# Performance work log

Hardware: AMD Instinct MI355X
Metric: run time of the kernel (lower is better)

## Reference

```python
import jax, jax.numpy as jnp
import numpy as np

B, N, C, NC = 16, 49, 512, 12  # batch, spatial tokens, channels, num AU classes
EPS = 1e-5


def bn(h, axes):
    # torch BatchNorm (training mode, gamma=1, beta=0): biased batch stats
    m = h.mean(axes, keepdims=True)
    v = h.var(axes, keepdims=True)
    return (h - m) * jax.lax.rsqrt(v + EPS)


def cross_attn(y, x, qw, qb, kw, kb, vw, vb):
    # CrossAttn: q from y, k/v from x; attention over the token (N) axis
    q = y @ qw.T + qb            # (..., N, C//2)
    k = x @ kw.T + kb
    v = x @ vw.T + vb            # (..., N, C)
    scale = (C // 2) ** -0.5
    attn = jax.nn.softmax(jnp.einsum('...ij,...kj->...ik', q, k) * scale, axis=-1)
    return attn @ v


def _gnn_block(x, edge, A, Bm, E, U, V):
    # One ME-GraphAU GCN message-passing block.
    # x: (B, NC, C) node feats; edge: (B, NC*NC, C), edge (i,j) stored at i*NC+j
    b = x.shape[0]
    Vix = x @ A.T   # gathered at end node j of each edge
    Vjx = x @ Bm.T  # gathered at start node i of each edge
    msg = (Vjx[:, :, None, :] + Vix[:, None, :, :]).reshape(b, NC * NC, C) + edge @ E.T
    edge = edge + jax.nn.relu(bn(msg, (0, 2)))              # bne: per-edge-slot stats
    e = jax.nn.sigmoid(edge).reshape(b, NC, NC, C)
    e = jax.nn.softmax(e, axis=2)                            # softmax over target j
    Ujx = x @ V.T                                            # start-node features
    agg = (e * Ujx[:, :, None, :]).sum(axis=1) / NC          # sum over source i -> node j
    xn = x @ U.T + agg
    x = jax.nn.relu(x + bn(xn, (0, 2)))                      # bnv: per-class stats
    return x, edge


def _forward(x, cls_w, cls_b, attn_qw, attn_qb, attn_kw, attn_kb, attn_vw, attn_vb,
             ep_w, ep_b, gnn_w, mlp_w1, mlp_b1, mlp_w2, mlp_b2, mlp_w3, mlp_b3,
             final_w, final_b):
    b = x.shape[0]
    # per-class LinearBlocks, batched: (B, NC, N, C)
    h = jnp.einsum('bnc,koc->bkno', x, cls_w) + cls_b[None, :, None, :]
    f_u = jax.nn.relu(bn(h, (0, 2)))           # each class has its own BN over (B, N)
    f_v = f_u.mean(-2)                          # (B, NC, C)

    # GEM edge extractor
    g = jnp.broadcast_to(x[:, None], (b, NC, N, C))
    feat = cross_attn(f_u, g, attn_qw[0], attn_qb[0], attn_kw[0], attn_kb[0], attn_vw[0], attn_vb[0])
    # feat_end[i*NC+j] = feat[i]; feat_start[i*NC+j] = feat[j]
    feat_end = jnp.broadcast_to(feat[:, :, None], (b, NC, NC, N, C)).reshape(b, NC * NC, N, C)
    feat_start = jnp.broadcast_to(feat[:, None, :], (b, NC, NC, N, C)).reshape(b, NC * NC, N, C)
    feat2 = cross_attn(feat_start, feat_end, attn_qw[1], attn_qb[1], attn_kw[1], attn_kb[1], attn_vw[1], attn_vb[1])
    edge = bn(feat2 @ ep_w.T + ep_b, (0, 2, 3))  # BatchNorm2d(NC*NC): stats over (B, N, C)
    f_e = edge.mean(-2)                           # (B, NC*NC, C)

    # two GCN message-passing blocks
    U1, V1, A1, B1, E1, U2, V2, A2, B2, E2 = gnn_w
    f_v, f_e = _gnn_block(f_v, f_e, A1, B1, E1, U1, V1)
    f_v, f_e = _gnn_block(f_v, f_e, A2, B2, E2, U2, V2)

    # vectorized pairwise class-link head (feed_type='vertex+edge'), pairs i<j in loop order
    iu, ju = np.triu_indices(NC, 1)
    edges = jnp.concatenate([f_e[:, iu * NC + ju], f_e[:, ju * NC + iu]], axis=-1)  # (B, 66, 2C)
    nodes = jnp.concatenate([f_v[:, iu], f_v[:, ju]], axis=-1)                       # (B, 66, 2C)

    def mlp(z, i):
        z = jax.nn.relu(z @ mlp_w1[i].T + mlp_b1[i])
        z = jax.nn.relu(z @ mlp_w2[i].T + mlp_b2[i])
        return z @ mlp_w3[i].T + mlp_b3[i]

    ed = mlp(edges, 0)
    nd = mlp(nodes, 1)
    return jnp.concatenate([ed, nd], axis=-1) @ final_w.T + final_b  # (B, 66, 4)


def setup_inputs() -> dict:
    key = jax.random.key(0)
    ks = jax.random.split(key, 12)

    def w(k, shape, fan_in):
        return jax.random.normal(k, shape, jnp.float32) * (2.0 / fan_in) ** 0.5

    return dict(
        x=jax.random.normal(ks[0], (B, N, C), jnp.float32),
        cls_w=w(ks[1], (NC, C, C), C),          # per-class Linear (out, in)
        cls_b=jnp.zeros((NC, C), jnp.float32),
        attn_qw=w(ks[2], (2, C // 2, C), C),    # [0]=FAM, [1]=ARM
        attn_qb=jnp.zeros((2, C // 2), jnp.float32),
        attn_kw=w(ks[3], (2, C // 2, C), C),
        attn_kb=jnp.zeros((2, C // 2), jnp.float32),
        attn_vw=w(ks[4], (2, C, C), C),
        attn_vb=jnp.zeros((2, C), jnp.float32),
        ep_w=w(ks[5], (C, C), C),               # GEM edge_proj
        ep_b=jnp.zeros((C,), jnp.float32),
        gnn_w=w(ks[6], (10, C, C), C),          # U1,V1,A1,B1,E1,U2,V2,A2,B2,E2 (no bias)
        mlp_w1=w(ks[7], (2, C, 2 * C), 2 * C),  # [0]=edge_fc_*, [1]=node_fc_*
        mlp_b1=jnp.zeros((2, C), jnp.float32),
        mlp_w2=w(ks[8], (2, C // 2, C), C),
        mlp_b2=jnp.zeros((2, C // 2), jnp.float32),
        mlp_w3=w(ks[9], (2, 4, C // 2), C // 2),
        mlp_b3=jnp.zeros((2, 4), jnp.float32),
        final_w=w(ks[10], (4, 8), 8),
        final_b=jnp.zeros((4,), jnp.float32),
    )


def reference(x, cls_w, cls_b, attn_qw, attn_qb, attn_kw, attn_kb, attn_vw, attn_vb,
              ep_w, ep_b, gnn_w, mlp_w1, mlp_b1, mlp_w2, mlp_b2, mlp_w3, mlp_b3,
              final_w, final_b):
    return _forward(x, cls_w, cls_b, attn_qw, attn_qb, attn_kw, attn_kb, attn_vw, attn_vb,
                    ep_w, ep_b, gnn_w, mlp_w1, mlp_b1, mlp_w2, mlp_b2, mlp_w3, mlp_b3,
                    final_w, final_b)
```

## Files before the change

kernel.cpp:

```cpp
#include <hip/hip_runtime.h>

#define BN_EPS 1e-5f

typedef float f32x4 __attribute__((ext_vector_type(4)));
typedef short s16x8 __attribute__((ext_vector_type(8)));

__device__ __forceinline__ short f2bf(float f) {
    unsigned u = __builtin_bit_cast(unsigned, f);
    u = (u + 0x7fffu + ((u >> 16) & 1u)) >> 16;
    return (short)u;
}

__global__ __launch_bounds__(256) void cvt_multi_kernel(
    const float* __restrict__ s0, const float* __restrict__ s1, const float* __restrict__ s2,
    const float* __restrict__ s3, const float* __restrict__ s4, const float* __restrict__ s5,
    const float* __restrict__ s6, const float* __restrict__ s7, const float* __restrict__ s8,
    short* __restrict__ d0, short* __restrict__ d1, short* __restrict__ d2,
    short* __restrict__ d3, short* __restrict__ d4, short* __restrict__ d5,
    short* __restrict__ d6, short* __restrict__ d7, short* __restrict__ d8)
{
    int idx = blockIdx.x * 256 + threadIdx.x;
    const float* src; short* dst; int local;
    if      (idx <   50176) { src = s0; dst = d0; local = idx; }
    else if (idx <  443392) { src = s1; dst = d1; local = idx -   50176; }
    else if (idx <  476160) { src = s2; dst = d2; local = idx -  443392; }
    else if (idx <  508928) { src = s3; dst = d3; local = idx -  476160; }
    else if (idx <  574464) { src = s4; dst = d4; local = idx -  508928; }
    else if (idx <  607232) { src = s5; dst = d5; local = idx -  574464; }
    else if (idx <  934912) { src = s6; dst = d6; local = idx -  607232; }
    else if (idx < 1065984) { src = s7; dst = d7; local = idx -  934912; }
    else if (idx < 1098752) { src = s8; dst = d8; local = idx - 1065984; }
    else return;
    const float4* s4p = reinterpret_cast<const float4*>(src) + (size_t)local * 2;
    float4 a = s4p[0], b = s4p[1];
    s16x8 v;
    v[0] = f2bf(a.x); v[1] = f2bf(a.y); v[2] = f2bf(a.z); v[3] = f2bf(a.w);
    v[4] = f2bf(b.x); v[5] = f2bf(b.y); v[6] = f2bf(b.z); v[7] = f2bf(b.w);
    reinterpret_cast<s16x8*>(dst)[local] = v;
}

template<int OMODE>
__global__ __launch_bounds__(256) void mfma_linear_kernel(
    const short* __restrict__ X, int Xstride,
    const short* __restrict__ W, int Wstride,
    const float* __restrict__ bias, int bstride,
    void* __restrict__ Yv, int Ystride,
    int R, int Cin, int Cout, int relu)
{
    const int mat = blockIdx.z;
    X += (size_t)mat * Xstride;
    W += (size_t)mat * Wstride;
    const float* bp = bias ? bias + mat * bstride : nullptr;
    float* Yf = (float*)Yv + (size_t)mat * Ystride;
    short* Ys = (short*)Yv + (size_t)mat * Ystride;

    const int r0 = blockIdx.y * 64;
    const int o0 = blockIdx.x * 64;

    __shared__ short As[64 * 40];
    __shared__ short Bs[64 * 40];

    const int tid = threadIdx.x;
    const int lane = tid & 63;
    const int wave = tid >> 6;
    const int wr = wave >> 1, wc = wave & 1;
    const int l15 = lane & 15;
    const int lk = lane >> 4;

    const int trow = tid >> 2;
    const int tseg = (tid & 3) * 8;

    f32x4 acc[2][2] = {};

    const int arow = r0 + trow;
    const bool aok = arow < R;
    const short* xrow = X + (size_t)arow * Cin + tseg;
    const short* wrow = W + (size_t)(o0 + trow) * Cin + tseg;

    for (int k0 = 0; k0 < Cin; k0 += 32) {
        s16x8 av = {};
        if (aok) av = *reinterpret_cast<const s16x8*>(xrow + k0);
        s16x8 bv = *reinterpret_cast<const s16x8*>(wrow + k0);
        *reinterpret_cast<s16x8*>(&As[trow * 40 + tseg]) = av;
        *reinterpret_cast<s16x8*>(&Bs[trow * 40 + tseg]) = bv;
        __syncthreads();

        s16x8 af[2], bf[2];
        #pragma unroll
        for (int mi = 0; mi < 2; mi++)
            af[mi] = *reinterpret_cast<const s16x8*>(&As[(wr * 32 + mi * 16 + l15) * 40 + lk * 8]);
        #pragma unroll
        for (int ni = 0; ni < 2; ni++)
            bf[ni] = *reinterpret_cast<const s16x8*>(&Bs[(wc * 32 + ni * 16 + l15) * 40 + lk * 8]);
        #pragma unroll
        for (int mi = 0; mi < 2; mi++)
            #pragma unroll
            for (int ni = 0; ni < 2; ni++)
                acc[mi][ni] = __builtin_amdgcn_mfma_f32_16x16x32_bf16(af[mi], bf[ni], acc[mi][ni], 0, 0, 0);
        __syncthreads();
    }

    #pragma unroll
    for (int mi = 0; mi < 2; mi++) {
        #pragma unroll
        for (int ni = 0; ni < 2; ni++) {
            int col = o0 + wc * 32 + ni * 16 + l15;
            int row0 = r0 + wr * 32 + mi * 16 + lk * 4;
            float bb = bp ? bp[col] : 0.f;
            #pragma unroll
            for (int r = 0; r < 4; r++) {
                int row = row0 + r;
                if (row < R) {
                    float v = acc[mi][ni][r] + bb;
                    if (relu) v = fmaxf(v, 0.f);
                    if (OMODE == 0) {
                        Yf[(size_t)row * Cout + col] = v;
                    } else if (OMODE == 1) {
                        Ys[(size_t)row * Cout + col] = f2bf(v);
                    } else {
                        int t = row / 49, n = row - t * 49;
                        Ys[((size_t)t * 512 + col) * 64 + n] = f2bf(v);
                    }
                }
            }
        }
    }
}

__global__ __launch_bounds__(256) void bn1_partial_kernel(
    const float* __restrict__ h, float* __restrict__ bsum, float* __restrict__ bsq)
{
    int k = blockIdx.x;
    int part = blockIdx.y;
    int tid = threadIdx.x;
    #pragma unroll
    for (int half = 0; half < 2; half++) {
        int o = tid + half * 256;
        const float* base = h + (size_t)k * 401408 + (size_t)part * 98 * 512 + o;
        float s = 0.f, sq = 0.f;
        #pragma unroll 7
        for (int bn = 0; bn < 98; bn++) {
            float v = base[bn * 512];
            s += v; sq += v * v;
        }
        atomicAdd(&bsum[k * 512 + o], s);
        atomicAdd(&bsq[k * 512 + o], sq);
    }
}

__global__ __launch_bounds__(256) void fu_fv_kernel(
    const float* __restrict__ h, const float* __restrict__ bsum,
    const float* __restrict__ bsq, short* __restrict__ fu_bf,
    float* __restrict__ f_v, short* __restrict__ fv_bf)
{
    int b = blockIdx.x;
    int k = blockIdx.y;
    int tid = threadIdx.x;
    #pragma unroll
    for (int half = 0; half < 2; half++) {
        int o = tid + half * 256;
        float mu = bsum[k * 512 + o] * (1.f / 784.f);
        float var = bsq[k * 512 + o] * (1.f / 784.f) - mu * mu;
        float rs = rsqrtf(var + BN_EPS);
        const float* base = h + (size_t)(k * 16 + b) * 49 * 512 + o;
        short* obase = fu_bf + (size_t)(k * 16 + b) * 49 * 512 + o;
        float acc = 0.f;
        #pragma unroll 7
        for (int n = 0; n < 49; n++) {
            float v = (base[n * 512] - mu) * rs;
            v = fmaxf(v, 0.f);
            obase[n * 512] = f2bf(v);
            acc += v;
        }
        float fvv = acc * (1.f / 49.f);
        f_v[(b * 12 + k) * 512 + o] = fvv;
        fv_bf[(b * 12 + k) * 512 + o] = f2bf(fvv);
    }
}

__global__ __launch_bounds__(256) void attn1_mfma_kernel(
    const short* __restrict__ q1,
    const short* __restrict__ k1,
    const short* __restrict__ v1T,
    short* __restrict__ feat)
{
    const int b = blockIdx.x, k = blockIdx.y;
    __shared__ float S[64 * 68];
    __shared__ short P[64 * 88];
    const int tid = threadIdx.x;
    const int lane = tid & 63, w = tid >> 6;
    const int l15 = lane & 15, lk = lane >> 4;

    for (int idx = tid; idx < 64 * 88; idx += 256) P[idx] = 0;
    const short* qb = q1 + (size_t)((k * 16 + b) * 49) * 256;
    const short* kb = k1 + (size_t)(b * 49) * 256;
    __syncthreads();

    {
        int qrow = w * 16 + l15; if (qrow > 48) qrow = 48;
        f32x4 sacc[4] = {};
        #pragma unroll
        for (int ks = 0; ks < 8; ks++) {
            s16x8 aq = *reinterpret_cast<const s16x8*>(qb + (size_t)qrow * 256 + ks * 32 + lk * 8);
            #pragma unroll
            for (int ni = 0; ni < 4; ni++) {
                int krow = ni * 16 + l15; if (krow > 48) krow = 48;
                s16x8 bk = *reinterpret_cast<const s16x8*>(kb + (size_t)krow * 256 + ks * 32 + lk * 8);
                sacc[ni] = __builtin_amdgcn_mfma_f32_16x16x32_bf16(aq, bk, sacc[ni], 0, 0, 0);
            }
        }
        #pragma unroll
        for (int ni = 0; ni < 4; ni++)
            #pragma unroll
            for (int r = 0; r < 4; r++)
                S[(w * 16 + lk * 4 + r) * 68 + ni * 16 + l15] = sacc[ni][r] * 0.0625f;
    }
    __syncthreads();

    if (tid < 196) {
        int qi = tid >> 2, sub = tid & 3;
        float ev[13];
        float m = -1e30f;
        #pragma unroll 13
        for (int t = 0; t < 13; t++) {
            int kk = sub + t * 4;
            ev[t] = (kk < 49) ? S[qi * 68 + kk] : -1e30f;
            m = fmaxf(m, ev[t]);
        }
        m = fmaxf(m, __shfl_xor(m, 1));
        m = fmaxf(m, __shfl_xor(m, 2));
        float s = 0.f;
        #pragma unroll 13
        for (int t = 0; t < 13; t++) { ev[t] = __expf(ev[t] - m); s += ev[t]; }
        s += __shfl_xor(s, 1);
        s += __shfl_xor(s, 2);
        float inv = 1.f / s;
        #pragma unroll 13
        for (int t = 0; t < 13; t++) {
            int kk = sub + t * 4;
            if (kk < 49) P[qi * 88 + kk] = f2bf(ev[t] * inv);
        }
    }
    __syncthreads();

    const short* vt = v1T + (size_t)b * 512 * 64;
    short* fb = feat + (size_t)((k * 16 + b) * 49) * 512;
    #pragma unroll
    for (int half = 0; half < 2; half++) {
        const int cb = half * 256 + w * 64;
        f32x4 pac[4][4] = {};
        #pragma unroll
        for (int ks = 0; ks < 2; ks++) {
            s16x8 bv[4];
            #pragma unroll
            for (int ni = 0; ni < 4; ni++) {
                int ch = cb + ni * 16 + l15;
                bv[ni] = *reinterpret_cast<const s16x8*>(vt + (size_t)ch * 64 + ks * 32 + lk * 8);
            }
            #pragma unroll
            for (int mi = 0; mi < 4; mi++) {
                s16x8 ap = *reinterpret_cast<const s16x8*>(&P[(mi * 16 + l15) * 88 + ks * 32 + lk * 8]);
                #pragma unroll
                for (int ni = 0; ni < 4; ni++)
                    pac[mi][ni] = __builtin_amdgcn_mfma_f32_16x16x32_bf16(ap, bv[ni], pac[mi][ni], 0, 0, 0);
            }
        }
        #pragma unroll
        for (int ni = 0; ni < 4; ni++) {
            int col = cb + ni * 16 + l15;
            #pragma unroll
            for (int mi = 0; mi < 4; mi++) {
                #pragma unroll
                for (int r = 0; r < 4; r++) {
                    int row = mi * 16 + lk * 4 + r;
                    if (row < 49)
                        fb[(size_t)row * 512 + col] = f2bf(pac[mi][ni][r]);
                }
            }
        }
    }
}

__global__ __launch_bounds__(256) void attn2_mfma_kernel(
    const short* __restrict__ q2,
    const short* __restrict__ k2,
    const short* __restrict__ w2vT,
    const float* __restrict__ ep_b,
    float* __restrict__ fe_raw,
    float* __restrict__ stats)
{
    const int b = blockIdx.x, i = blockIdx.y;
    __shared__ short Vs[512 * 64];
    __shared__ float S[64 * 68];
    __shared__ short P[64 * 88];
    const int tid = threadIdx.x;
    const int lane = tid & 63, w = tid >> 6;
    const int l15 = lane & 15, lk = lane >> 4;

    {
        const float4* src = reinterpret_cast<const float4*>(w2vT + (size_t)((i * 16 + b) * 512) * 64);
        float4* dst = reinterpret_cast<float4*>(Vs);
        #pragma unroll
        for (int it = 0; it < 16; it++) {
            int c = tid + it * 256;
            int ch = c >> 3, c8 = c & 7;
            dst[(ch << 3) | (c8 ^ (ch & 7))] = src[c];
        }
        for (int idx = tid; idx < 64 * 88; idx += 256) P[idx] = 0;
    }
    const short* kb = k2 + (size_t)((i * 16 + b) * 49) * 256;
    __syncthreads();

    for (int j = 0; j < 12; j++) {
        const short* qb = q2 + (size_t)((j * 16 + b) * 49) * 256;
        {
            int qrow = w * 16 + l15; if (qrow > 48) qrow = 48;
            f32x4 sacc[4] = {};
            #pragma unroll
            for (int ks = 0; ks < 8; ks++) {
                s16x8 aq = *reinterpret_cast<const s16x8*>(qb + (size_t)qrow * 256 + ks * 32 + lk * 8);
                #pragma unroll
                for (int ni = 0; ni < 4; ni++) {
                    int krow = ni * 16 + l15; if (krow > 48) krow = 48;
                    s16x8 bk = *reinterpret_cast<const s16x8*>(kb + (size_t)krow * 256 + ks * 32 + lk * 8);
                    sacc[ni] = __builtin_amdgcn_mfma_f32_16x16x32_bf16(aq, bk, sacc[ni], 0, 0, 0);
                }
            }
            #pragma unroll
            for (int ni = 0; ni < 4; ni++)
                #pragma unroll
                for (int r = 0; r < 4; r++)
                    S[(w * 16 + lk * 4 + r) * 68 + ni * 16 + l15] = sacc[ni][r] * 0.0625f;
        }
        __syncthreads();

        if (tid < 196) {
            int qi = tid >> 2, sub = tid & 3;
            float ev[13];
            float m = -1e30f;
            #pragma unroll 13
            for (int t = 0; t < 13; t++) {
                int kk = sub + t * 4;
                ev[t] = (kk < 49) ? S[qi * 68 + kk] : -1e30f;
                m = fmaxf(m, ev[t]);
            }
            m = fmaxf(m, __shfl_xor(m, 1));
            m = fmaxf(m, __shfl_xor(m, 2));
            float s = 0.f;
            #pragma unroll 13
            for (int t = 0; t < 13; t++) { ev[t] = __expf(ev[t] - m); s += ev[t]; }
            s += __shfl_xor(s, 1);
            s += __shfl_xor(s, 2);
            float inv = 1.f / s;
            #pragma unroll 13
            for (int t = 0; t < 13; t++) {
                int kk = sub + t * 4;
                if (kk < 49) P[qi * 88 + kk] = f2bf(ev[t] * inv);
            }
        }
        __syncthreads();

        const int slot = i * 12 + j;
        float tot = 0.f, csq = 0.f;
        #pragma unroll
        for (int half = 0; half < 2; half++) {
            const int cb = half * 256 + w * 64;
            f32x4 pac[4][4] = {};
            #pragma unroll
            for (int ks = 0; ks < 2; ks++) {
                s16x8 bv[4];
                #pragma unroll
                for (int ni = 0; ni < 4; ni++) {
                    int ch = cb + ni * 16 + l15;
                    int boff = ((ch * 64 + ks * 32 + lk * 8) * 2) ^ ((ch & 7) << 4);
                    bv[ni] = *reinterpret_cast<const s16x8*>(reinterpret_cast<const char*>(Vs) + boff);
                }
                #pragma unroll
                for (int mi = 0; mi < 4; mi++) {
                    s16x8 ap = *reinterpret_cast<const s16x8*>(&P[(mi * 16 + l15) * 88 + ks * 32 + lk * 8]);
                    #pragma unroll
                    for (int ni = 0; ni < 4; ni++)
                        pac[mi][ni] = __builtin_amdgcn_mfma_f32_16x16x32_bf16(ap, bv[ni], pac[mi][ni], 0, 0, 0);
                }
            }
            #pragma unroll
            for (int ni = 0; ni < 4; ni++) {
                int col = cb + ni * 16 + l15;
                float bias = ep_b[col];
                float cs = 0.f;
                #pragma unroll
                for (int mi = 0; mi < 4; mi++) {
                    #pragma unroll
                    for (int r = 0; r < 4; r++) {
                        int row = mi * 16 + lk * 4 + r;
                        if (row < 49) {
                            float sv = pac[mi][ni][r] + bias;
                            cs += sv; csq += sv * sv;
                        }
                    }
                }
                tot += cs;
                cs += __shfl_xor(cs, 16);
                cs += __shfl_xor(cs, 32);
                if (lk == 0)
                    fe_raw[((size_t)b * 144 + slot) * 512 + col] = cs * (1.f / 49.f);
            }
        }
        tot += __shfl_xor(tot, 1);  tot += __shfl_xor(tot, 2);  tot += __shfl_xor(tot, 4);
        tot += __shfl_xor(tot, 8);  tot += __shfl_xor(tot, 16); tot += __shfl_xor(tot, 32);
        csq += __shfl_xor(csq, 1);  csq += __shfl_xor(csq, 2);  csq += __shfl_xor(csq, 4);
        csq += __shfl_xor(csq, 8);  csq += __shfl_xor(csq, 16); csq += __shfl_xor(csq, 32);
        if (lane == 0) {
            atomicAdd(&stats[slot * 2], tot);
            atomicAdd(&stats[slot * 2 + 1], csq);
        }
    }
}

__global__ __launch_bounds__(256) void edge_fin_kernel(
    const float* __restrict__ stats, float* __restrict__ fe, short* __restrict__ fe_bf)
{
    int s = blockIdx.x;
    const float inv = 1.f / 401408.f;
    float mu = stats[s * 2] * inv;
    float var = stats[s * 2 + 1] * inv - mu * mu;
    float rs = rsqrtf(var + BN_EPS);
    int tid = threadIdx.x;
    for (int b = 0; b < 16; b++) {
        float* p = fe + (b * 144 + s) * 512;
        short* pb = fe_bf + (b * 144 + s) * 512;
        #pragma unroll
        for (int half = 0; half < 2; half++) {
            int c = tid + half * 256;
            float nv = (p[c] - mu) * rs;
            p[c] = nv;
            pb[c] = f2bf(nv);
        }
    }
}

__global__ __launch_bounds__(256) void gnn_edge_kernel(
    const float* __restrict__ nodeproj,
    const float* __restrict__ eE,
    float* __restrict__ fe, short* __restrict__ fe_bf)
{
    int s = blockIdx.x;
    int i = s / 12, j = s - i * 12;
    int tid = threadIdx.x;
    const float* Vix = nodeproj + 2 * 98304;
    const float* Vjx = nodeproj + 3 * 98304;
    __shared__ float red[256];
    float msg[32];
    float sum = 0.f, sq = 0.f;
    int idx = 0;
    for (int b = 0; b < 16; b++) {
        #pragma unroll
        for (int half = 0; half < 2; half++) {
            int c = tid + half * 256;
            float v = Vjx[(b * 12 + i) * 512 + c] + Vix[(b * 12 + j) * 512 + c]
                    + eE[(b * 144 + s) * 512 + c];
            msg[idx++] = v;
            sum += v; sq += v * v;
        }
    }
    red[tid] = sum; __syncthreads();
    for (int t = 128; t > 0; t >>= 1) { if (tid < t) red[tid] += red[tid + t]; __syncthreads(); }
    float tsum = red[0]; __syncthreads();
    red[tid] = sq; __syncthreads();
    for (int t = 128; t > 0; t >>= 1) { if (tid < t) red[tid] += red[tid + t]; __syncthreads(); }
    float tsq = red[0];
    float mu = tsum * (1.f / 8192.f);
    float var = tsq * (1.f / 8192.f) - mu * mu;
    float rs = rsqrtf(var + BN_EPS);
    idx = 0;
    for (int b = 0; b < 16; b++) {
        #pragma unroll
        for (int half = 0; half < 2; half++) {
            int c = tid + half * 256;
            int o = (b * 144 + s) * 512 + c;
            float v = fmaxf((msg[idx++] - mu) * rs, 0.f);
            float nv = fe[o] + v;
            fe[o] = nv;
            fe_bf[o] = f2bf(nv);
        }
    }
}

__global__ __launch_bounds__(256) void gnn_agg_kernel(
    const float* __restrict__ fe,
    const float* __restrict__ nodeproj,
    float* __restrict__ xn_agg)
{
    int b = blockIdx.x;
    int i = blockIdx.y;
    int tid = threadIdx.x;
    const float* Ujx = nodeproj + 98304;
    #pragma unroll
    for (int half = 0; half < 2; half++) {
        int c = tid + half * 256;
        float sg[12];
        float m = -1e30f;
        #pragma unroll
        for (int j = 0; j < 12; j++) {
            float e = fe[(b * 144 + i * 12 + j) * 512 + c];
            float sv = 1.f / (1.f + __expf(-e));
            sg[j] = sv;
            m = fmaxf(m, sv);
        }
        float ssum = 0.f;
        #pragma unroll
        for (int j = 0; j < 12; j++) { float evv = __expf(sg[j] - m); sg[j] = evv; ssum += evv; }
        float wgt = Ujx[(b * 12 + i) * 512 + c] / ssum;
        #pragma unroll
        for (int j = 0; j < 12; j++)
            atomicAdd(&xn_agg[(b * 12 + j) * 512 + c], sg[j] * wgt);
    }
}

__global__ __launch_bounds__(256) void gnn_node_kernel(
    const float* __restrict__ xn_agg, const float* __restrict__ nodeproj,
    float* __restrict__ fv, short* __restrict__ fv_bf)
{
    int k = blockIdx.x;
    int tid = threadIdx.x;
    const float* Ux = nodeproj;
    __shared__ float red[256];
    float vals[32];
    float sum = 0.f, sq = 0.f;
    int idx = 0;
    for (int b = 0; b < 16; b++) {
        #pragma unroll
        for (int half = 0; half < 2; half++) {
            int c = tid + half * 256;
            int o = (b * 12 + k) * 512 + c;
            float v = Ux[o] + xn_agg[o] * (1.f / 12.f);
            vals[idx++] = v;
            sum += v; sq += v * v;
        }
    }
    red[tid] = sum; __syncthreads();
    for (int t = 128; t > 0; t >>= 1) { if (tid < t) red[tid] += red[tid + t]; __syncthreads(); }
    float tsum = red[0]; __syncthreads();
    red[tid] = sq; __syncthreads();
    for (int t = 128; t > 0; t >>= 1) { if (tid < t) red[tid] += red[tid + t]; __syncthreads(); }
    float tsq = red[0];
    float mu = tsum * (1.f / 8192.f);
    float var = tsq * (1.f / 8192.f) - mu * mu;
    float rs = rsqrtf(var + BN_EPS);
    idx = 0;
    for (int b = 0; b < 16; b++) {
        #pragma unroll
        for (int half = 0; half < 2; half++) {
            int c = tid + half * 256;
            int o = (b * 12 + k) * 512 + c;
            float v = (vals[idx++] - mu) * rs;
            float nv = fmaxf(fv[o] + v, 0.f);
            fv[o] = nv;
            fv_bf[o] = f2bf(nv);
        }
    }
}

__global__ __launch_bounds__(256) void pair_gather_kernel(
    const float* __restrict__ fe, const float* __restrict__ fv, short* __restrict__ pairX)
{
    int p = blockIdx.x;
    int b = blockIdx.y;
    int tid = threadIdx.x;
    int i = 0, rem = p;
    while (rem >= 11 - i) { rem -= 11 - i; i++; }
    int j = i + 1 + rem;
    short* e_out = pairX + (size_t)(b * 66 + p) * 1024;
    short* n_out = pairX + (size_t)1056 * 1024 + (size_t)(b * 66 + p) * 1024;
    const float* fe_ij = fe + (b * 144 + i * 12 + j) * 512;
    const float* fe_ji = fe + (b * 144 + j * 12 + i) * 512;
    const float* fv_i = fv + (b * 12 + i) * 512;
    const float* fv_j = fv + (b * 12 + j) * 512;
    #pragma unroll
    for (int half = 0; half < 2; half++) {
        int c = tid + half * 256;
        e_out[c] = f2bf(fe_ij[c]);
        e_out[512 + c] = f2bf(fe_ji[c]);
        n_out[c] = f2bf(fv_i[c]);
        n_out[512 + c] = f2bf(fv_j[c]);
    }
}

__global__ __launch_bounds__(256) void mlp3_kernel(
    const float* __restrict__ X,
    const float* __restrict__ w3,
    const float* __restrict__ b3,
    float* __restrict__ Y)
{
    int idx = blockIdx.x * 256 + threadIdx.x;
    if (idx >= 8448) return;
    int o = idx & 3;
    int r = (idx >> 2) % 1056;
    int m = idx / (4 * 1056);
    const float* x = X + (m * 1056 + r) * 256;
    const float* w = w3 + (m * 4 + o) * 256;
    float s = b3[m * 4 + o];
    #pragma unroll 8
    for (int c = 0; c < 256; c++) s += x[c] * w[c];
    Y[idx] = s;
}

__global__ __launch_bounds__(256) void final_kernel(
    const float* __restrict__ mid3,
    const float* __restrict__ fw,
    const float* __restrict__ fb,
    float* __restrict__ out)
{
    int idx = blockIdx.x * 256 + threadIdx.x;
    if (idx >= 4224) return;
    int o = idx & 3;
    int r = idx >> 2;
    const float* ed = mid3 + r * 4;
    const float* nd = mid3 + 1056 * 4 + r * 4;
    float s = fb[o];
    #pragma unroll
    for (int q = 0; q < 4; q++) s += ed[q] * fw[o * 8 + q];
    #pragma unroll
    for (int q = 0; q < 4; q++) s += nd[q] * fw[o * 8 + 4 + q];
    out[idx] = s;
}

extern "C" void kernel_launch(void* const* d_in, const int* in_sizes, int n_in,
                              void* d_out, int out_size, void* d_ws, size_t ws_size,
                              hipStream_t stream)
{
    const float* x      = (const float*)d_in[0];
    const float* cls_w  = (const float*)d_in[1];
    const float* cls_b  = (const float*)d_in[2];
    const float* qw     = (const float*)d_in[3];
    const float* qb     = (const float*)d_in[4];
    const float* kw     = (const float*)d_in[5];
    const float* kb     = (const float*)d_in[6];
    const float* vw     = (const float*)d_in[7];
    const float* vb     = (const float*)d_in[8];
    const float* ep_w   = (const float*)d_in[9];
    const float* ep_b   = (const float*)d_in[10];
    const float* gnn_w  = (const float*)d_in[11];
    const float* mlp_w1 = (const float*)d_in[12];
    const float* mlp_b1 = (const float*)d_in[13];
    const float* mlp_w2 = (const float*)d_in[14];
    const float* mlp_b2 = (const float*)d_in[15];
    const float* mlp_w3 = (const float*)d_in[16];
    const float* mlp_b3 = (const float*)d_in[17];
    const float* fin_w  = (const float*)d_in[18];
    const float* fin_b  = (const float*)d_in[19];
    float* out = (float*)d_out;
    float* ws = (float*)d_ws;

    float* A      = ws;
    float* q1b    = A + 4816896;
    float* k1b    = q1b + 2408448;
    float* v1b    = k1b + 200704;
    float* Bb     = v1b + 401408;
    float* Cb     = Bb + 3145728;
    float* fv     = Cb + 2408448;
    float* fvbf_f = fv + 98304;
    float* bn1m   = fvbf_f + 49152;
    float* bn1r   = bn1m + 6144;
    float* fe     = bn1r + 6144;
    float* febf_f = fe + 1179648;
    float* stats  = febf_f + 589824;
    float* xbf_f  = stats + 288;
    float* cwbf_f = xbf_f + 200704;
    float* qwbf_f = cwbf_f + 1572864;
    float* kwbf_f = qwbf_f + 131072;
    float* vwbf_f = kwbf_f + 131072;
    float* ewbf_f = vwbf_f + 262144;
    float* gwbf_f = ewbf_f + 131072;
    float* m1bf_f = gwbf_f + 1310720;
    float* m2bf_f = m1bf_f + 524288;

    short* xbf   = (short*)xbf_f;
    short* cwbf  = (short*)cwbf_f;
    short* qwbf  = (short*)qwbf_f;
    short* kwbf  = (short*)kwbf_f;
    short* vwbf  = (short*)vwbf_f;
    short* ewbf  = (short*)ewbf_f;
    short* gwbf  = (short*)gwbf_f;
    short* m1wbf = (short*)m1bf_f;
    short* m2wbf = (short*)m2bf_f;

    short* fubf   = (short*)Cb;
    short* featbf = (short*)Bb;
    short* q2bf   = (short*)A;
    short* k2bf   = (short*)A + 2408448;
    short* v2bf   = (short*)Cb;
    short* w2vT   = (short*)Bb;
    short* fvbf   = (short*)fvbf_f;
    short* febf   = (short*)febf_f;
    short* q1bfb  = (short*)q1b;
    short* k1bfb  = (short*)k1b;
    short* v1T    = (short*)v1b;

    float* nodeproj = Cb;
    float* eE       = Cb + 393216;
    float* xn       = Cb + 1572864;
    short* pairXbf  = (short*)Cb;
    short* mid1bf   = (short*)Cb + 2162688;
    float* mid2     = Cb + 1622016;
    float* mid3     = Cb + 2162688;

    cvt_multi_kernel<<<4293, 256, 0, stream>>>(
        x, cls_w, qw, kw, vw, ep_w, gnn_w, mlp_w1, mlp_w2,
        xbf, cwbf, qwbf, kwbf, vwbf, ewbf, gwbf, m1wbf, m2wbf);

    mfma_linear_kernel<0><<<dim3(8, 13, 12), 256, 0, stream>>>(xbf, 0, cwbf, 262144, cls_b, 512,
                                                               A, 401408, 784, 512, 512, 0);
    hipMemsetAsync(bn1m, 0, 2 * 6144 * sizeof(float), stream);
    bn1_partial_kernel<<<dim3(12, 8), 256, 0, stream>>>(A, bn1m, bn1r);
    fu_fv_kernel<<<dim3(16, 12), 256, 0, stream>>>(A, bn1m, bn1r, fubf, fv, fvbf);
    mfma_linear_kernel<1><<<dim3(4, 147, 1), 256, 0, stream>>>(fubf, 0, qwbf, 0, qb, 0,
                                                               q1bfb, 0, 9408, 512, 256, 0);
    mfma_linear_kernel<1><<<dim3(4, 13, 1), 256, 0, stream>>>(xbf, 0, kwbf, 0, kb, 0,
                                                              k1bfb, 0, 784, 512, 256, 0);
    hipMemsetAsync(v1T, 0, (size_t)16 * 512 * 64 * sizeof(short), stream);
    mfma_linear_kernel<2><<<dim3(8, 13, 1), 256, 0, stream>>>(xbf, 0, vwbf, 0, vb, 0,
                                                              v1T, 0, 784, 512, 512, 0);
    attn1_mfma_kernel<<<dim3(16, 12), 256, 0, stream>>>(q1bfb, k1bfb, v1T, featbf);
    mfma_linear_kernel<1><<<dim3(4, 147, 1), 256, 0, stream>>>(featbf, 0, qwbf + 131072, 0, qb + 256, 0,
                                                               q2bf, 0, 9408, 512, 256, 0);
    mfma_linear_kernel<1><<<dim3(4, 147, 1), 256, 0, stream>>>(featbf, 0, kwbf + 131072, 0, kb + 256, 0,
                                                               k2bf, 0, 9408, 512, 256, 0);
    mfma_linear_kernel<1><<<dim3(8, 147, 1), 256, 0, stream>>>(featbf, 0, vwbf + 262144, 0, vb + 512, 0,
                                                               v2bf, 0, 9408, 512, 512, 0);
    hipMemsetAsync(w2vT, 0, (size_t)12 * 16 * 512 * 64 * sizeof(short), stream);
    mfma_linear_kernel<2><<<dim3(8, 147, 1), 256, 0, stream>>>(v2bf, 0, ewbf, 0, nullptr, 0,
                                                               w2vT, 0, 9408, 512, 512, 0);
    hipMemsetAsync(stats, 0, 288 * sizeof(float), stream);
    attn2_mfma_kernel<<<dim3(16, 12), 256, 0, stream>>>(q2bf, k2bf, w2vT, ep_b, fe, stats);
    edge_fin_kernel<<<144, 256, 0, stream>>>(stats, fe, febf);

    for (int blk = 0; blk < 2; blk++) {
        const short* gw = gwbf + blk * 5 * 262144;
        mfma_linear_kernel<0><<<dim3(8, 3, 4), 256, 0, stream>>>(fvbf, 0, gw, 262144, nullptr, 0,
                                                                 nodeproj, 98304, 192, 512, 512, 0);
        mfma_linear_kernel<0><<<dim3(8, 36, 1), 256, 0, stream>>>(febf, 0, gw + 4 * 262144, 0, nullptr, 0,
                                                                  eE, 0, 2304, 512, 512, 0);
        gnn_edge_kernel<<<144, 256, 0, stream>>>(nodeproj, eE, fe, febf);
        hipMemsetAsync(xn, 0, 98304 * sizeof(float), stream);
        gnn_agg_kernel<<<dim3(16, 12), 256, 0, stream>>>(fe, nodeproj, xn);
        gnn_node_kernel<<<12, 256, 0, stream>>>(xn, nodeproj, fv, fvbf);
    }

    pair_gather_kernel<<<dim3(66, 16), 256, 0, stream>>>(fe, fv, pairXbf);
    mfma_linear_kernel<1><<<dim3(8, 17, 2), 256, 0, stream>>>(pairXbf, 1081344, m1wbf, 524288, mlp_b1, 512,
                                                              mid1bf, 540672, 1056, 1024, 512, 1);
    mfma_linear_kernel<0><<<dim3(4, 17, 2), 256, 0, stream>>>(mid1bf, 540672, m2wbf, 131072, mlp_b2, 256,
                                                              mid2, 270336, 1056, 512, 256, 1);
    mlp3_kernel<<<33, 256, 0, stream>>>(mid2, mlp_w3, mlp_b3, mid3);
    final_kernel<<<17, 256, 0, stream>>>(mid3, fin_w, fin_b, out);
}
```

Measured before the change: 432.7 us.

## Fuse BN stats into class GEMM, fold memsets into kernels, merge head

Computes the per-class BatchNorm sum and sum-of-squares in the class-linear GEMM epilogue with atomics, so the separate bn1_partial pass that re-read the large activation is gone. Several hipMemsetAsync calls are folded into existing kernels: cvt zeros v1T, bn1 and stats, edge_fin zeros xn, and gnn_node resets xn after reading it. The mlp3 and final kernels are merged into one head kernel. This cuts launch count and one full read of h, at the cost of more atomics in the GEMM epilogue and more redundant dot products in the head.

Result: slower. 451.0 us (+4.2%).

```diff
diff --git a/kernel.cpp b/kernel.cpp
--- a/kernel.cpp
+++ b/kernel.cpp
@@ -17,9 +17,27 @@
     const float* __restrict__ s6, const float* __restrict__ s7, const float* __restrict__ s8,
     short* __restrict__ d0, short* __restrict__ d1, short* __restrict__ d2,
     short* __restrict__ d3, short* __restrict__ d4, short* __restrict__ d5,
-    short* __restrict__ d6, short* __restrict__ d7, short* __restrict__ d8)
+    short* __restrict__ d6, short* __restrict__ d7, short* __restrict__ d8,
+    short* __restrict__ z_v1T, float* __restrict__ z_bn, float* __restrict__ z_st)
 {
     int idx = blockIdx.x * 256 + threadIdx.x;
+    if (idx >= 1098752) {
+        if (idx < 1164288) {
+            s16x8 z = {};
+            reinterpret_cast<s16x8*>(z_v1T)[idx - 1098752] = z;
+        } else if (idx < 1165824) {
+            int l = idx - 1164288;
+            float4 z4 = {0.f, 0.f, 0.f, 0.f};
+            float4* p = reinterpret_cast<float4*>(z_bn) + (size_t)l * 2;
+            p[0] = z4; p[1] = z4;
+        } else if (idx < 1165860) {
+            int l = idx - 1165824;
+            float4 z4 = {0.f, 0.f, 0.f, 0.f};
+            float4* p = reinterpret_cast<float4*>(z_st) + (size_t)l * 2;
+            p[0] = z4; p[1] = z4;
+        }
+        return;
+    }
     const float* src; short* dst; int local;
     if      (idx <   50176) { src = s0; dst = d0; local = idx; }
     else if (idx <  443392) { src = s1; dst = d1; local = idx -   50176; }
@@ -29,8 +47,7 @@
     else if (idx <  607232) { src = s5; dst = d5; local = idx -  574464; }
     else if (idx <  934912) { src = s6; dst = d6; local = idx -  607232; }
     else if (idx < 1065984) { src = s7; dst = d7; local = idx -  934912; }
-    else if (idx < 1098752) { src = s8; dst = d8; local = idx - 1065984; }
-    else return;
+    else                    { src = s8; dst = d8; local = idx - 1065984; }
     const float4* s4p = reinterpret_cast<const float4*>(src) + (size_t)local * 2;
     float4 a = s4p[0], b = s4p[1];
     s16x8 v;
@@ -45,7 +62,8 @@
     const short* __restrict__ W, int Wstride,
     const float* __restrict__ bias, int bstride,
     void* __restrict__ Yv, int Ystride,
-    int R, int Cin, int Cout, int relu)
+    int R, int Cin, int Cout, int relu,
+    float* __restrict__ bsum, float* __restrict__ bsq)
 {
     const int mat = blockIdx.z;
     X += (size_t)mat * Xstride;
@@ -98,6 +116,35 @@
             for (int ni = 0; ni < 2; ni++)
                 acc[mi][ni] = __builtin_amdgcn_mfma_f32_16x16x32_bf16(af[mi], bf[ni], acc[mi][ni], 0, 0, 0);
         __syncthreads();
+    }
+
+    if (OMODE == 3) {
+        #pragma unroll
+        for (int ni = 0; ni < 2; ni++) {
+            int col = o0 + wc * 32 + ni * 16 + l15;
+            float bb = bp ? bp[col] : 0.f;
+            float cs = 0.f, cq = 0.f;
+            #pragma unroll
+            for (int mi = 0; mi < 2; mi++) {
+                int row0 = r0 + wr * 32 + mi * 16 + lk * 4;
+                #pragma unroll
+                for (int r = 0; r < 4; r++) {
+                    int row = row0 + r;
+                    if (row < R) {
+                        float v = acc[mi][ni][r] + bb;
+                        Yf[(size_t)row * Cout + col] = v;
+                        cs += v; cq += v * v;
+                    }
+                }
+            }
+            cs += __shfl_xor(cs, 16); cs += __shfl_xor(cs, 32);
+            cq += __shfl_xor(cq, 16); cq += __shfl_xor(cq, 32);
+            if (lk == 0) {
+                atomicAdd(&bsum[(size_t)mat * 512 + col], cs);
+                atomicAdd(&bsq[(size_t)mat * 512 + col], cq);
+            }
+        }
+        return;
     }
 
     #pragma unroll
@@ -124,27 +171,6 @@
                 }
             }
         }
-    }
-}
-
-__global__ __launch_bounds__(256) void bn1_partial_kernel(
-    const float* __restrict__ h, float* __restrict__ bsum, float* __restrict__ bsq)
-{
-    int k = blockIdx.x;
-    int part = blockIdx.y;
-    int tid = threadIdx.x;
-    #pragma unroll
-    for (int half = 0; half < 2; half++) {
-        int o = tid + half * 256;
-        const float* base = h + (size_t)k * 401408 + (size_t)part * 98 * 512 + o;
-        float s = 0.f, sq = 0.f;
-        #pragma unroll 7
-        for (int bn = 0; bn < 98; bn++) {
-            float v = base[bn * 512];
-            s += v; sq += v * v;
-        }
-        atomicAdd(&bsum[k * 512 + o], s);
-        atomicAdd(&bsq[k * 512 + o], sq);
     }
 }
 
@@ -418,14 +444,20 @@
 }
 
 __global__ __launch_bounds__(256) void edge_fin_kernel(
-    const float* __restrict__ stats, float* __restrict__ fe, short* __restrict__ fe_bf)
+    const float* __restrict__ stats, float* __restrict__ fe, short* __restrict__ fe_bf,
+    float* __restrict__ xnz)
 {
     int s = blockIdx.x;
+    int tid = threadIdx.x;
+    int gt = s * 256 + tid;
+    if (gt < 24576) {
+        float4 z4 = {0.f, 0.f, 0.f, 0.f};
+        reinterpret_cast<float4*>(xnz)[gt] = z4;
+    }
     const float inv = 1.f / 401408.f;
     float mu = stats[s * 2] * inv;
     float var = stats[s * 2 + 1] * inv - mu * mu;
     float rs = rsqrtf(var + BN_EPS);
-    int tid = threadIdx.x;
     for (int b = 0; b < 16; b++) {
         float* p = fe + (b * 144 + s) * 512;
         short* pb = fe_bf + (b * 144 + s) * 512;
@@ -518,7 +550,7 @@
 }
 
 __global__ __launch_bounds__(256) void gnn_node_kernel(
-    const float* __restrict__ xn_agg, const float* __restrict__ nodeproj,
+    float* __restrict__ xn_agg, const float* __restrict__ nodeproj,
     float* __restrict__ fv, short* __restrict__ fv_bf)
 {
     int k = blockIdx.x;
@@ -534,6 +566,7 @@
             int c = tid + half * 256;
             int o = (b * 12 + k) * 512 + c;
             float v = Ux[o] + xn_agg[o] * (1.f / 12.f);
+            xn_agg[o] = 0.f;
             vals[idx++] = v;
             sum += v; sq += v * v;
         }
@@ -586,27 +619,10 @@
     }
 }
 
-__global__ __launch_bounds__(256) void mlp3_kernel(
-    const float* __restrict__ X,
+__global__ __launch_bounds__(256) void head_kernel(
+    const float* __restrict__ mid2,
     const float* __restrict__ w3,
     const float* __restrict__ b3,
-    float* __restrict__ Y)
-{
-    int idx = blockIdx.x * 256 + threadIdx.x;
-    if (idx >= 8448) return;
-    int o = idx & 3;
-    int r = (idx >> 2) % 1056;
-    int m = idx / (4 * 1056);
-    const float* x = X + (m * 1056 + r) * 256;
-    const float* w = w3 + (m * 4 + o) * 256;
-    float s = b3[m * 4 + o];
-    #pragma unroll 8
-    for (int c = 0; c < 256; c++) s += x[c] * w[c];
-    Y[idx] = s;
-}
-
-__global__ __launch_bounds__(256) void final_kernel(
-    const float* __restrict__ mid3,
     const float* __restrict__ fw,
     const float* __restrict__ fb,
     float* __restrict__ out)
@@ -615,13 +631,19 @@
     if (idx >= 4224) return;
     int o = idx & 3;
     int r = idx >> 2;
-    const float* ed = mid3 + r * 4;
-    const float* nd = mid3 + 1056 * 4 + r * 4;
     float s = fb[o];
     #pragma unroll
-    for (int q = 0; q < 4; q++) s += ed[q] * fw[o * 8 + q];
-    #pragma unroll
-    for (int q = 0; q < 4; q++) s += nd[q] * fw[o * 8 + 4 + q];
+    for (int m = 0; m < 2; m++) {
+        const float* xrow = mid2 + (size_t)(m * 1056 + r) * 256;
+        #pragma unroll
+        for (int q = 0; q < 4; q++) {
+            const float* w = w3 + (m * 4 + q) * 256;
+            float d = b3[m * 4 + q];
+            #pragma unroll 8
+            for (int c = 0; c < 256; c++) d += xrow[c] * w[c];
+            s += d * fw[o * 8 + m * 4 + q];
+        }
+    }
     out[idx] = s;
 }
 
@@ -703,55 +725,61 @@
     short* pairXbf  = (short*)Cb;
     short* mid1bf   = (short*)Cb + 2162688;
     float* mid2     = Cb + 1622016;
-    float* mid3     = Cb + 2162688;
-
-    cvt_multi_kernel<<<4293, 256, 0, stream>>>(
+
+    cvt_multi_kernel<<<4555, 256, 0, stream>>>(
         x, cls_w, qw, kw, vw, ep_w, gnn_w, mlp_w1, mlp_w2,
-        xbf, cwbf, qwbf, kwbf, vwbf, ewbf, gwbf, m1wbf, m2wbf);
-
-    mfma_linear_kernel<0><<<dim3(8, 13, 12), 256, 0, stream>>>(xbf, 0, cwbf, 262144, cls_b, 512,
-                                                               A, 401408, 784, 512, 512, 0);
-    hipMemsetAsync(bn1m, 0, 2 * 6144 * sizeof(float), stream);
-    bn1_partial_kernel<<<dim3(12, 8), 256, 0, stream>>>(A, bn1m, bn1r);
+        xbf, cwbf, qwbf, kwbf, vwbf, ewbf, gwbf, m1wbf, m2wbf,
+        v1T, bn1m, stats);
+
+    mfma_linear_kernel<3><<<dim3(8, 13, 12), 256, 0, stream>>>(xbf, 0, cwbf, 262144, cls_b, 512,
+                                                               A, 401408, 784, 512, 512, 0,
+                                                               bn1m, bn1r);
     fu_fv_kernel<<<dim3(16, 12), 256, 0, stream>>>(A, bn1m, bn1r, fubf, fv, fvbf);
     mfma_linear_kernel<1><<<dim3(4, 147, 1), 256, 0, stream>>>(fubf, 0, qwbf, 0, qb, 0,
-                                                               q1bfb, 0, 9408, 512, 256, 0);
+                                                               q1bfb, 0, 9408, 512, 256, 0,
+                                                               nullptr, nullptr);
     mfma_linear_kernel<1><<<dim3(4, 13, 1), 256, 0, stream>>>(xbf, 0, kwbf, 0, kb, 0,
-                                                              k1bfb, 0, 784, 512, 256, 0);
-    hipMemsetAsync(v1T, 0, (size_t)16 * 512 * 64 * sizeof(short), stream);
+                                                              k1bfb, 0, 784, 512, 256, 0,
+                                                              nullptr, nullptr);
     mfma_linear_kernel<2><<<dim3(8, 13, 1), 256, 0, stream>>>(xbf, 0, vwbf, 0, vb, 0,
-                                                              v1T, 0, 784, 512, 512, 0);
+                                                              v1T, 0, 784, 512, 512, 0,
+                                                              nullptr, nullptr);
     attn1_mfma_kernel<<<dim3(16, 12), 256, 0, stream>>>(q1bfb, k1bfb, v1T, featbf);
     mfma_linear_kernel<1><<<dim3(4, 147, 1), 256, 0, stream>>>(featbf, 0, qwbf + 131072, 0, qb + 256, 0,
-                                                               q2bf, 0, 9408, 512, 256, 0);
+                                                               q2bf, 0, 9408, 512, 256, 0,
+                                                               nullptr, nullptr);
     mfma_linear_kernel<1><<<dim3(4, 147, 1), 256, 0, stream>>>(featbf, 0, kwbf + 131072, 0, kb + 256, 0,
-                                                               k2bf, 0, 9408, 512, 256, 0);
+                                                               k2bf, 0, 9408, 512, 256, 0,
+                                                               nullptr, nullptr);
     mfma_linear_kernel<1><<<dim3(8, 147, 1), 256, 0, stream>>>(featbf, 0, vwbf + 262144, 0, vb + 512, 0,
-                                                               v2bf, 0, 9408, 512, 512, 0);
+                                                               v2bf, 0, 9408, 512, 512, 0,
+                                                               nullptr, nullptr);
     hipMemsetAsync(w2vT, 0, (size_t)12 * 16 * 512 * 64 * sizeof(short), stream);
     mfma_linear_kernel<2><<<dim3(8, 147, 1), 256, 0, stream>>>(v2bf, 0, ewbf, 0, nullptr, 0,
-                                                               w2vT, 0, 9408, 512, 512, 0);
-    hipMemsetAsync(stats, 0, 288 * sizeof(float), stream);
+                                                               w2vT, 0, 9408, 512, 512, 0,
+                                                               nullptr, nullptr);
     attn2_mfma_kernel<<<dim3(16, 12), 256, 0, stream>>>(q2bf, k2bf, w2vT, ep_b, fe, stats);
-    edge_fin_kernel<<<144, 256, 0, stream>>>(stats, fe, febf);
+    edge_fin_kernel<<<144, 256, 0, stream>>>(stats, fe, febf, xn);
 
     for (int blk = 0; blk < 2; blk++) {
         const short* gw = gwbf + blk * 5 * 262144;
         mfma_linear_kernel<0><<<dim3(8, 3, 4), 256, 0, stream>>>(fvbf, 0, gw, 262144, nullptr, 0,
-                                                                 nodeproj, 98304, 192, 512, 512, 0);
+                                                                 nodeproj, 98304, 192, 512, 512, 0,
+                                                                 nullptr, nullptr);
         mfma_linear_kernel<0><<<dim3(8, 36, 1), 256, 0, stream>>>(febf, 0, gw + 4 * 262144, 0, nullptr, 0,
-                                                                  eE, 0, 2304, 512, 512, 0);
+                                                                  eE, 0, 2304, 512, 512, 0,
+                                                                  nullptr, nullptr);
         gnn_edge_kernel<<<144, 256, 0, stream>>>(nodeproj, eE, fe, febf);
-        hipMemsetAsync(xn, 0, 98304 * sizeof(float), stream);
         gnn_agg_kernel<<<dim3(16, 12), 256, 0, stream>>>(fe, nodeproj, xn);
         gnn_node_kernel<<<12, 256, 0, stream>>>(xn, nodeproj, fv, fvbf);
     }
 
     pair_gather_kernel<<<dim3(66, 16), 256, 0, stream>>>(fe, fv, pairXbf);
     mfma_linear_kernel<1><<<dim3(8, 17, 2), 256, 0, stream>>>(pairXbf, 1081344, m1wbf, 524288, mlp_b1, 512,
-                                                              mid1bf, 540672, 1056, 1024, 512, 1);
+                                                              mid1bf, 540672, 1056, 1024, 512, 1,
+                                                              nullptr, nullptr);
     mfma_linear_kernel<0><<<dim3(4, 17, 2), 256, 0, stream>>>(mid1bf, 540672, m2wbf, 131072, mlp_b2, 256,
-                                                              mid2, 270336, 1056, 512, 256, 1);
-    mlp3_kernel<<<33, 256, 0, stream>>>(mid2, mlp_w3, mlp_b3, mid3);
-    final_kernel<<<17, 256, 0, stream>>>(mid3, fin_w, fin_b, out);
-}
+                                                              mid2, 270336, 1056, 512, 256, 1,
+                                                              nullptr, nullptr);
+    head_kernel<<<17, 256, 0, stream>>>(mid2, mlp_w3, mlp_b3, fin_w, fin_b, out);
+}
```
